# Performance work log

Hardware: AMD Instinct MI355X
Metric: run time of the kernel (lower is better)

## Reference

```python
import jax, jax.numpy as jnp
import numpy as np

B = 8
C = 256
NS = [16384, 4096, 1024, 256, 1]  # point-pyramid sizes per level
D = 3                              # coordinate dim
EPS = (1e-06, 1e-06, 1e-06, 1e-06, 1e-06)


def _pm_level(x, coords_c, coords_n, idx, p_i, eps_i):
    """One hierarchical gather-weighted power-mean pooling step.
    x: (B, C, N)  coords_c: (B, N, D)  coords_n: (B, Nn, D)  idx: (B, N) in [0, Nn).
    Returns pooled features (B, C, Nn)."""
    Bq, Cq, N = x.shape
    Nn = coords_n.shape[1]
    Dd = coords_c.shape[-1]
    # gather parent coords for each child, delta to parent
    cn = jnp.take_along_axis(coords_n, idx[:, :, None], axis=1)            # (B,N,D)
    delta = coords_c - cn                                                   # (B,N,D)
    # per-parent max/min of delta (scatter_max / scatter_min)
    smax = jax.vmap(lambda d, ix: jax.ops.segment_max(d, ix, num_segments=Nn))(delta, idx)
    smin = jax.vmap(lambda d, ix: jax.ops.segment_min(d, ix, num_segments=Nn))(delta, idx)
    pos_ub = jnp.maximum(smax, 0.0)   # clamp(min=0)
    neg_lb = jnp.minimum(smin, 0.0)   # clamp(max=0)
    # gather bounds back to children, pick by sign of delta
    pos_g = jnp.take_along_axis(pos_ub, idx[:, :, None], axis=1)
    neg_g = jnp.take_along_axis(neg_lb, idx[:, :, None], axis=1)
    inuse = jnp.where(delta >= 0.0, pos_g, neg_g)
    w = 1.0 - jnp.abs(delta) / (jnp.abs(inuse) + 1e-6)                      # (B,N,D)
    # split channels across the D coordinate weights: [q, q, ..., q+r]
    q, r = Cq // Dd, Cq % Dd
    reps = np.asarray([q] * (Dd - 1) + [q + r])
    w_c = jnp.repeat(w, reps, axis=-1, total_repeat_length=Cq)              # (B,N,C)
    x_pow = jnp.maximum(x, eps_i) ** p_i                                    # (B,C,N)
    xw = x_pow.transpose(0, 2, 1) * w_c                                     # (B,N,C)
    # scatter_sum of weighted powers and of weights, per parent cell
    xw_s = jax.vmap(lambda a, ix: jax.ops.segment_sum(a, ix, num_segments=Nn))(xw, idx)   # (B,Nn,C)
    w_s = jax.vmap(lambda a, ix: jax.ops.segment_sum(a, ix, num_segments=Nn))(w_c, idx)   # (B,Nn,C)
    nxt = (xw_s / (w_s + 1e-6)) ** (1.0 / p_i)
    return nxt.transpose(0, 2, 1)                                           # (B,C,Nn)


def setup_inputs() -> dict:
    key = jax.random.key(0)
    ks = jax.random.split(key, 16)
    x = jax.random.normal(ks[0], (B, C, NS[0]), dtype=jnp.float32)
    coords = [jax.random.normal(ks[1 + i], (B, NS[i], D), dtype=jnp.float32) for i in range(5)]
    idxs = []
    for i in range(4):
        # every parent gets ~NS[i]/NS[i+1] children; permute per batch for irregular access
        base = jnp.arange(NS[i], dtype=jnp.int32) % NS[i + 1]
        bk = jax.random.split(ks[6 + i], B)
        idxs.append(jax.vmap(lambda k: jax.random.permutation(k, base))(bk))
    p = jnp.full((5,), 3.0, dtype=jnp.float32)
    return {"x": x,
            "idx0": idxs[0], "idx1": idxs[1], "idx2": idxs[2], "idx3": idxs[3],
            "coords0": coords[0], "coords1": coords[1], "coords2": coords[2],
            "coords3": coords[3], "coords4": coords[4],
            "p": p}


def reference(x, idx0, idx1, idx2, idx3, coords0, coords1, coords2, coords3, coords4, p):
    idxs = (idx0, idx1, idx2, idx3)
    coords = (coords0, coords1, coords2, coords3, coords4)
    cur = x
    for i in range(4):
        cur = _pm_level(cur, coords[i], coords[i + 1], idxs[i], p[i], EPS[i])
    return cur[..., 0]  # squeeze (B,C,1) -> (B,C)
```

## Files before the change

kernel.cpp:

```cpp
#include <hip/hip_runtime.h>
#include <math.h>

constexpr int B  = 8;
constexpr int C  = 256;
constexpr int Q  = 85;
constexpr int NS0 = 16384, NS1 = 4096, NS2 = 1024, NS3 = 256;
constexpr int PAR = NS1 + NS2 + NS3;
constexpr int SLT = NS0 + NS1 + NS2;

__device__ __forceinline__ int cdim(int c) {
    int d = c / Q;
    return d > 2 ? 2 : d;
}

__global__ void invert_fused_kernel(const int* __restrict__ idx0,
                                    const int* __restrict__ idx1,
                                    const int* __restrict__ idx2,
                                    const float* __restrict__ c0,
                                    const float* __restrict__ c1,
                                    const float* __restrict__ c2,
                                    const float* __restrict__ c3,
                                    const float* __restrict__ c4,
                                    unsigned* __restrict__ cnt,
                                    float4*   __restrict__ dslot,
                                    float*    __restrict__ w3,
                                    float*    __restrict__ z4) {
    __shared__ float sm[3][256];
    __shared__ float sn[3][256];

    if (blockIdx.y == 3) {
        if (blockIdx.x >= 8) return;
        int b = blockIdx.x;
        int n = threadIdx.x;

        float pc0 = c4[b * 3 + 0], pc1 = c4[b * 3 + 1], pc2 = c4[b * 3 + 2];
        const float* cp = &c3[((size_t)(b * 256 + n)) * 3];
        float d0 = cp[0] - pc0, d1 = cp[1] - pc1, d2 = cp[2] - pc2;
        sm[0][n] = d0; sm[1][n] = d1; sm[2][n] = d2;
        sn[0][n] = d0; sn[1][n] = d1; sn[2][n] = d2;
        __syncthreads();
        for (int s = 128; s > 0; s >>= 1) {
            if (n < s) {
#pragma unroll
                for (int d = 0; d < 3; ++d) {
                    sm[d][n] = fmaxf(sm[d][n], sm[d][n + s]);
                    sn[d][n] = fminf(sn[d][n], sn[d][n + s]);
                }
            }
            __syncthreads();
        }
        float pos0 = fmaxf(sm[0][0], 0.f), pos1 = fmaxf(sm[1][0], 0.f), pos2 = fmaxf(sm[2][0], 0.f);
        float neg0 = fminf(sn[0][0], 0.f), neg1 = fminf(sn[1][0], 0.f), neg2 = fminf(sn[2][0], 0.f);
        __syncthreads();

        float w0 = 1.f - fabsf(d0) / (fabsf(d0 >= 0.f ? pos0 : neg0) + 1e-6f);
        float w1 = 1.f - fabsf(d1) / (fabsf(d1 >= 0.f ? pos1 : neg1) + 1e-6f);
        float w2 = 1.f - fabsf(d2) / (fabsf(d2 >= 0.f ? pos2 : neg2) + 1e-6f);
        float* wp = &w3[((size_t)(b * 256 + n)) * 3];
        wp[0] = w0; wp[1] = w1; wp[2] = w2;

        sm[0][n] = w0; sm[1][n] = w1; sm[2][n] = w2;
        __syncthreads();
        for (int s = 128; s > 0; s >>= 1) {
            if (n < s) {
#pragma unroll
                for (int d = 0; d < 3; ++d) sm[d][n] += sm[d][n + s];
            }
            __syncthreads();
        }
        if (n == 0) {
            z4[b * 3 + 0] = sm[0][0];
            z4[b * 3 + 1] = sm[1][0];
            z4[b * 3 + 2] = sm[2][0];
        }
        return;
    }

    int lvl = blockIdx.y;
    const int*   idx = (lvl == 0) ? idx0 : (lvl == 1 ? idx1 : idx2);
    const float* cc  = (lvl == 0) ? c0   : (lvl == 1 ? c1   : c2);
    const float* cn  = (lvl == 0) ? c1   : (lvl == 1 ? c2   : c3);
    int N  = (lvl == 0) ? NS0 : (lvl == 1 ? NS1 : NS2);
    int Nn = (lvl == 0) ? NS1 : (lvl == 1 ? NS2 : NS3);
    int cbase = (lvl == 0) ? 0 : (lvl == 1 ? NS1 : NS1 + NS2);
    int sbase = (lvl == 0) ? 0 : (lvl == 1 ? NS0 : NS0 + NS1);

    int t = blockIdx.x * blockDim.x + threadIdx.x;
    if (t >= B * N) return;
    int b = t / N;
    int n = t - b * N;
    int j = idx[t];
    int pj = b * Nn + j;

    unsigned o = atomicAdd(&cnt[(size_t)b * PAR + cbase + j], 1u);
    int slot = (int)(o & 3u);

    float4 dv;
    dv.x = cc[(size_t)t * 3 + 0] - cn[(size_t)pj * 3 + 0];
    dv.y = cc[(size_t)t * 3 + 1] - cn[(size_t)pj * 3 + 1];
    dv.z = cc[(size_t)t * 3 + 2] - cn[(size_t)pj * 3 + 2];
    dv.w = __int_as_float(n);
    dslot[((size_t)b * SLT + sbase + (size_t)j * 4) + slot] = dv;
}

__global__ void weights3_kernel(const float4* __restrict__ dslot,
                                float* __restrict__ w0,
                                float* __restrict__ w1,
                                float* __restrict__ w2,
                                float* __restrict__ z1,
                                float* __restrict__ z2,
                                float* __restrict__ z3)
{
    int lvl = blockIdx.y;
    int N  = (lvl == 0) ? NS0 : (lvl == 1 ? NS1 : NS2);
    int Nn = (lvl == 0) ? NS1 : (lvl == 1 ? NS2 : NS3);
    int sbase = (lvl == 0) ? 0 : (lvl == 1 ? NS0 : NS0 + NS1);
    float* w = (lvl == 0) ? w0 : (lvl == 1 ? w1 : w2);
    float* z = (lvl == 0) ? z1 : (lvl == 1 ? z2 : z3);

    int t = blockIdx.x * blockDim.x + threadIdx.x;
    if (t >= B * Nn) return;
    int b = t / Nn;
    int j = t - b * Nn;

    const float4* dp = &dslot[(size_t)b * SLT + sbase + (size_t)j * 4];
    float4 ch0 = dp[0], ch1 = dp[1], ch2 = dp[2], ch3 = dp[3];

    float mx0 = fmaxf(fmaxf(ch0.x, ch1.x), fmaxf(ch2.x, ch3.x));
    float mn0 = fminf(fminf(ch0.x, ch1.x), fminf(ch2.x, ch3.x));
    float mx1 = fmaxf(fmaxf(ch0.y, ch1.y), fmaxf(ch2.y, ch3.y));
    float mn1 = fminf(fminf(ch0.y, ch1.y), fminf(ch2.y, ch3.y));
    float mx2 = fmaxf(fmaxf(ch0.z, ch1.z), fmaxf(ch2.z, ch3.z));
    float mn2 = fminf(fminf(ch0.z, ch1.z), fminf(ch2.z, ch3.z));

    float pos0 = fmaxf(mx0, 0.f), neg0 = fminf(mn0, 0.f);
    float pos1 = fmaxf(mx1, 0.f), neg1 = fminf(mn1, 0.f);
    float pos2 = fmaxf(mx2, 0.f), neg2 = fminf(mn2, 0.f);

    float zz0 = 0.f, zz1 = 0.f, zz2 = 0.f;
    float4 chs[4] = {ch0, ch1, ch2, ch3};
#pragma unroll
    for (int k = 0; k < 4; ++k) {
        float d0 = chs[k].x, d1 = chs[k].y, d2 = chs[k].z;
        int   n  = __float_as_int(chs[k].w);
        float wv0 = 1.f - fabsf(d0) / (fabsf(d0 >= 0.f ? pos0 : neg0) + 1e-6f);
        float wv1 = 1.f - fabsf(d1) / (fabsf(d1 >= 0.f ? pos1 : neg1) + 1e-6f);
        float wv2 = 1.f - fabsf(d2) / (fabsf(d2 >= 0.f ? pos2 : neg2) + 1e-6f);
        float* wp = &w[((size_t)b * N + n) * 3];
        wp[0] = wv0; wp[1] = wv1; wp[2] = wv2;
        zz0 += wv0; zz1 += wv1; zz2 += wv2;
    }
    float* zp = &z[(size_t)t * 3];
    zp[0] = zz0; zp[1] = zz1; zp[2] = zz2;
}

__global__ void wchain_kernel(const int* __restrict__ idx0,
                              const int* __restrict__ idx1,
                              const int* __restrict__ idx2,
                              const float* __restrict__ w0,
                              const float* __restrict__ z1,
                              const float* __restrict__ w1,
                              const float* __restrict__ z2,
                              const float* __restrict__ w2,
                              const float* __restrict__ z3,
                              const float* __restrict__ w3,
                              const float* __restrict__ z4,
                              float* __restrict__ Wn) {
    int t = blockIdx.x * blockDim.x + threadIdx.x;
    if (t >= B * NS0) return;
    int b = t / NS0;
    int n = t - b * NS0;
    int a1 = idx0[t];            int p1 = b * NS1 + a1;
    int a2 = idx1[p1];           int p2 = b * NS2 + a2;
    int a3 = idx2[p2];           int p3 = b * NS3 + a3;
#pragma unroll
    for (int d = 0; d < 3; ++d) {
        float v = w0[(size_t)t * 3 + d]  / (z1[(size_t)p1 * 3 + d] + 1e-6f);
        v *=      w1[(size_t)p1 * 3 + d] / (z2[(size_t)p2 * 3 + d] + 1e-6f);
        v *=      w2[(size_t)p2 * 3 + d] / (z3[(size_t)p3 * 3 + d] + 1e-6f);
        v *=      w3[(size_t)p3 * 3 + d] / (z4[b * 3 + d] + 1e-6f);
        Wn[((size_t)(b * 3 + d)) * NS0 + n] = v;
    }
}

__global__ void final_kernel(const float* __restrict__ x,
                             const float* __restrict__ Wn,
                             float* __restrict__ out,
                             const float* __restrict__ p_arr) {
    __shared__ float sred[256];
    int bc = blockIdx.x;
    int b = bc / C;
    int c = bc - b * C;
    int d = cdim(c);
    float p = p_arr[0];
    bool p3 = (p == 3.0f);

    const float4* xr = (const float4*)(x + (size_t)bc * NS0);
    const float4* wr = (const float4*)(Wn + ((size_t)(b * 3 + d)) * NS0);

    float acc = 0.f;
#pragma unroll 4
    for (int i = threadIdx.x; i < NS0 / 4; i += 256) {
        float4 xv = xr[i];
        float4 wv = wr[i];
        float v0 = fmaxf(xv.x, 1e-6f);
        float v1 = fmaxf(xv.y, 1e-6f);
        float v2 = fmaxf(xv.z, 1e-6f);
        float v3 = fmaxf(xv.w, 1e-6f);
        float s0 = p3 ? v0 * v0 * v0 : powf(v0, p);
        float s1 = p3 ? v1 * v1 * v1 : powf(v1, p);
        float s2 = p3 ? v2 * v2 * v2 : powf(v2, p);
        float s3 = p3 ? v3 * v3 * v3 : powf(v3, p);
        acc = fmaf(s0, wv.x, acc);
        acc = fmaf(s1, wv.y, acc);
        acc = fmaf(s2, wv.z, acc);
        acc = fmaf(s3, wv.w, acc);
    }
    sred[threadIdx.x] = acc;
    __syncthreads();
    for (int s = 128; s > 0; s >>= 1) {
        if (threadIdx.x < s) sred[threadIdx.x] += sred[threadIdx.x + s];
        __syncthreads();
    }
    if (threadIdx.x == 0) {
        float t = sred[0];
        out[bc] = p3 ? cbrtf(t) : powf(t, 1.0f / p);
    }
}

extern "C" void kernel_launch(void* const* d_in, const int* in_sizes, int n_in,
                              void* d_out, int out_size, void* d_ws, size_t ws_size,
                              hipStream_t stream) {
    const float* x      = (const float*)d_in[0];
    const int*   idx0   = (const int*)d_in[1];
    const int*   idx1   = (const int*)d_in[2];
    const int*   idx2   = (const int*)d_in[3];
    const float* coords0 = (const float*)d_in[5];
    const float* coords1 = (const float*)d_in[6];
    const float* coords2 = (const float*)d_in[7];
    const float* coords3 = (const float*)d_in[8];
    const float* coords4 = (const float*)d_in[9];
    const float* p = (const float*)d_in[10];

    char* ws = (char*)d_ws;
    size_t off = 0;
    auto alloc = [&](size_t bytes) -> void* {
        off = (off + 255) & ~(size_t)255;
        void* r = ws + off;
        off += bytes;
        return r;
    };

    unsigned* cnt  = (unsigned*)alloc((size_t)B * PAR * sizeof(unsigned));
    float4*  dslot = (float4*)alloc((size_t)B * SLT * sizeof(float4));
    float* w0 = (float*)alloc((size_t)B * NS0 * 3 * sizeof(float));
    float* w1 = (float*)alloc((size_t)B * NS1 * 3 * sizeof(float));
    float* w2 = (float*)alloc((size_t)B * NS2 * 3 * sizeof(float));
    float* w3 = (float*)alloc((size_t)B * NS3 * 3 * sizeof(float));
    float* z1 = (float*)alloc((size_t)B * NS1 * 3 * sizeof(float));
    float* z2 = (float*)alloc((size_t)B * NS2 * 3 * sizeof(float));
    float* z3 = (float*)alloc((size_t)B * NS3 * 3 * sizeof(float));
    float* z4 = (float*)alloc((size_t)B * 1   * 3 * sizeof(float));
    float* Wn = (float*)alloc((size_t)B * 3 * NS0 * sizeof(float));

    dim3 ig((B * NS0 + 255) / 256, 4);
    invert_fused_kernel<<<ig, 256, 0, stream>>>(
        idx0, idx1, idx2, coords0, coords1, coords2, coords3, coords4,
        cnt, dslot, w3, z4);

    dim3 wg((B * NS1 + 255) / 256, 3);
    weights3_kernel<<<wg, 256, 0, stream>>>(dslot, w0, w1, w2, z1, z2, z3);

    wchain_kernel<<<(B * NS0 + 255) / 256, 256, 0, stream>>>(
        idx0, idx1, idx2, w0, z1, w1, z2, w2, z3, w3, z4, Wn);

    final_kernel<<<B * C, 256, 0, stream>>>(x, Wn, (float*)d_out, p);
}
```

Baseline: 50.19 us.

## Fuse leaf-level weight computation into Wn chain, drop w0/z1 buffers

```diff
diff --git a/kernel.cpp b/kernel.cpp
--- a/kernel.cpp
+++ b/kernel.cpp
@@ -103,20 +103,18 @@
     dslot[((size_t)b * SLT + sbase + (size_t)j * 4) + slot] = dv;
 }
 
-__global__ void weights3_kernel(const float4* __restrict__ dslot,
-                                float* __restrict__ w0,
-                                float* __restrict__ w1,
-                                float* __restrict__ w2,
-                                float* __restrict__ z1,
-                                float* __restrict__ z2,
-                                float* __restrict__ z3)
+__global__ void weights_mid_kernel(const float4* __restrict__ dslot,
+                                   float* __restrict__ w1,
+                                   float* __restrict__ w2,
+                                   float* __restrict__ z2,
+                                   float* __restrict__ z3)
 {
-    int lvl = blockIdx.y;
-    int N  = (lvl == 0) ? NS0 : (lvl == 1 ? NS1 : NS2);
-    int Nn = (lvl == 0) ? NS1 : (lvl == 1 ? NS2 : NS3);
-    int sbase = (lvl == 0) ? 0 : (lvl == 1 ? NS0 : NS0 + NS1);
-    float* w = (lvl == 0) ? w0 : (lvl == 1 ? w1 : w2);
-    float* z = (lvl == 0) ? z1 : (lvl == 1 ? z2 : z3);
+    int lvl = blockIdx.y + 1;
+    int N  = (lvl == 1) ? NS1 : NS2;
+    int Nn = (lvl == 1) ? NS2 : NS3;
+    int sbase = (lvl == 1) ? NS0 : NS0 + NS1;
+    float* w = (lvl == 1) ? w1 : w2;
+    float* z = (lvl == 1) ? z2 : z3;
 
     int t = blockIdx.x * blockDim.x + threadIdx.x;
     if (t >= B * Nn) return;
@@ -154,32 +152,74 @@
     zp[0] = zz0; zp[1] = zz1; zp[2] = zz2;
 }
 
-__global__ void wchain_kernel(const int* __restrict__ idx0,
-                              const int* __restrict__ idx1,
-                              const int* __restrict__ idx2,
-                              const float* __restrict__ w0,
-                              const float* __restrict__ z1,
+__global__ void leafwn_kernel(const float4* __restrict__ dslot,
+                              const int*   __restrict__ idx1,
+                              const int*   __restrict__ idx2,
                               const float* __restrict__ w1,
+                              const float* __restrict__ w2,
+                              const float* __restrict__ w3,
                               const float* __restrict__ z2,
-                              const float* __restrict__ w2,
                               const float* __restrict__ z3,
-                              const float* __restrict__ w3,
                               const float* __restrict__ z4,
                               float* __restrict__ Wn) {
     int t = blockIdx.x * blockDim.x + threadIdx.x;
-    if (t >= B * NS0) return;
-    int b = t / NS0;
-    int n = t - b * NS0;
-    int a1 = idx0[t];            int p1 = b * NS1 + a1;
-    int a2 = idx1[p1];           int p2 = b * NS2 + a2;
-    int a3 = idx2[p2];           int p3 = b * NS3 + a3;
-#pragma unroll
-    for (int d = 0; d < 3; ++d) {
-        float v = w0[(size_t)t * 3 + d]  / (z1[(size_t)p1 * 3 + d] + 1e-6f);
-        v *=      w1[(size_t)p1 * 3 + d] / (z2[(size_t)p2 * 3 + d] + 1e-6f);
-        v *=      w2[(size_t)p2 * 3 + d] / (z3[(size_t)p3 * 3 + d] + 1e-6f);
-        v *=      w3[(size_t)p3 * 3 + d] / (z4[b * 3 + d] + 1e-6f);
-        Wn[((size_t)(b * 3 + d)) * NS0 + n] = v;
+    if (t >= B * NS1) return;
+    int b = t / NS1;
+    int j = t - b * NS1;
+
+    const float4* dp = &dslot[(size_t)b * SLT + (size_t)j * 4];
+    float4 ch0 = dp[0], ch1 = dp[1], ch2 = dp[2], ch3 = dp[3];
+
+    float mx0 = fmaxf(fmaxf(ch0.x, ch1.x), fmaxf(ch2.x, ch3.x));
+    float mn0 = fminf(fminf(ch0.x, ch1.x), fminf(ch2.x, ch3.x));
+    float mx1 = fmaxf(fmaxf(ch0.y, ch1.y), fmaxf(ch2.y, ch3.y));
+    float mn1 = fminf(fminf(ch0.y, ch1.y), fminf(ch2.y, ch3.y));
+    float mx2 = fmaxf(fmaxf(ch0.z, ch1.z), fmaxf(ch2.z, ch3.z));
+    float mn2 = fminf(fminf(ch0.z, ch1.z), fminf(ch2.z, ch3.z));
+
+    float pos0 = fmaxf(mx0, 0.f), neg0 = fminf(mn0, 0.f);
+    float pos1 = fmaxf(mx1, 0.f), neg1 = fminf(mn1, 0.f);
+    float pos2 = fmaxf(mx2, 0.f), neg2 = fminf(mn2, 0.f);
+
+    float wv0[4], wv1[4], wv2[4];
+    int   nid[4];
+    float zz0 = 0.f, zz1 = 0.f, zz2 = 0.f;
+    float4 chs[4] = {ch0, ch1, ch2, ch3};
+#pragma unroll
+    for (int k = 0; k < 4; ++k) {
+        float d0 = chs[k].x, d1 = chs[k].y, d2 = chs[k].z;
+        nid[k] = __float_as_int(chs[k].w);
+        wv0[k] = 1.f - fabsf(d0) / (fabsf(d0 >= 0.f ? pos0 : neg0) + 1e-6f);
+        wv1[k] = 1.f - fabsf(d1) / (fabsf(d1 >= 0.f ? pos1 : neg1) + 1e-6f);
+        wv2[k] = 1.f - fabsf(d2) / (fabsf(d2 >= 0.f ? pos2 : neg2) + 1e-6f);
+        zz0 += wv0[k]; zz1 += wv1[k]; zz2 += wv2[k];
+    }
+
+    int a2 = idx1[t];
+    int a3 = idx2[(size_t)b * NS2 + a2];
+    size_t i1 = (size_t)t * 3;
+    size_t i2 = ((size_t)b * NS2 + a2) * 3;
+    size_t i3 = ((size_t)b * NS3 + a3) * 3;
+    float U0 = w1[i1 + 0] / (z2[i2 + 0] + 1e-6f) * w2[i2 + 0] / (z3[i3 + 0] + 1e-6f)
+             * w3[i3 + 0] / (z4[b * 3 + 0] + 1e-6f);
+    float U1v = w1[i1 + 1] / (z2[i2 + 1] + 1e-6f) * w2[i2 + 1] / (z3[i3 + 1] + 1e-6f)
+             * w3[i3 + 1] / (z4[b * 3 + 1] + 1e-6f);
+    float U2 = w1[i1 + 2] / (z2[i2 + 2] + 1e-6f) * w2[i2 + 2] / (z3[i3 + 2] + 1e-6f)
+             * w3[i3 + 2] / (z4[b * 3 + 2] + 1e-6f);
+
+    float r0 = U0 / (zz0 + 1e-6f);
+    float r1 = U1v / (zz1 + 1e-6f);
+    float r2 = U2 / (zz2 + 1e-6f);
+
+    float* Wb0 = Wn + ((size_t)(b * 3 + 0)) * NS0;
+    float* Wb1 = Wn + ((size_t)(b * 3 + 1)) * NS0;
+    float* Wb2 = Wn + ((size_t)(b * 3 + 2)) * NS0;
+#pragma unroll
+    for (int k = 0; k < 4; ++k) {
+        int n = nid[k];
+        Wb0[n] = wv0[k] * r0;
+        Wb1[n] = wv1[k] * r1;
+        Wb2[n] = wv2[k] * r2;
     }
 }
 
@@ -199,7 +239,7 @@
     const float4* wr = (const float4*)(Wn + ((size_t)(b * 3 + d)) * NS0);
 
     float acc = 0.f;
-#pragma unroll 4
+#pragma unroll 8
     for (int i = threadIdx.x; i < NS0 / 4; i += 256) {
         float4 xv = xr[i];
         float4 wv = wr[i];
@@ -253,11 +293,9 @@
 
     unsigned* cnt  = (unsigned*)alloc((size_t)B * PAR * sizeof(unsigned));
     float4*  dslot = (float4*)alloc((size_t)B * SLT * sizeof(float4));
-    float* w0 = (float*)alloc((size_t)B * NS0 * 3 * sizeof(float));
     float* w1 = (float*)alloc((size_t)B * NS1 * 3 * sizeof(float));
     float* w2 = (float*)alloc((size_t)B * NS2 * 3 * sizeof(float));
     float* w3 = (float*)alloc((size_t)B * NS3 * 3 * sizeof(float));
-    float* z1 = (float*)alloc((size_t)B * NS1 * 3 * sizeof(float));
     float* z2 = (float*)alloc((size_t)B * NS2 * 3 * sizeof(float));
     float* z3 = (float*)alloc((size_t)B * NS3 * 3 * sizeof(float));
     float* z4 = (float*)alloc((size_t)B * 1   * 3 * sizeof(float));
@@ -268,11 +306,11 @@
         idx0, idx1, idx2, coords0, coords1, coords2, coords3, coords4,
         cnt, dslot, w3, z4);
 
-    dim3 wg((B * NS1 + 255) / 256, 3);
-    weights3_kernel<<<wg, 256, 0, stream>>>(dslot, w0, w1, w2, z1, z2, z3);
-
-    wchain_kernel<<<(B * NS0 + 255) / 256, 256, 0, stream>>>(
-        idx0, idx1, idx2, w0, z1, w1, z2, w2, z3, w3, z4, Wn);
+    dim3 mg((B * NS2 + 255) / 256, 2);
+    weights_mid_kernel<<<mg, 256, 0, stream>>>(dslot, w1, w2, z2, z3);
+
+    leafwn_kernel<<<(B * NS1 + 255) / 256, 256, 0, stream>>>(
+        dslot, idx1, idx2, w1, w2, w3, z2, z3, z4, Wn);
 
     final_kernel<<<B * C, 256, 0, stream>>>(x, Wn, (float*)d_out, p);
 }
```

Measured after the change: 50.86 us. About the same (+1.3%).
